# Kernel optimization log

Measured on AMD Instinct MI355X. Metric: run time of the kernel, lower is better.

Reference implementation:

```python
import jax, jax.numpy as jnp
import numpy as np


def _one_sided_chamfer(a, b):
    # a: [B, N, 3], b: [B, M, 3]
    # squared pairwise distances via ||a||^2 + ||b||^2 - 2 a.b
    a2 = jnp.sum(a * a, axis=-1)              # [B, N]
    b2 = jnp.sum(b * b, axis=-1)              # [B, M]
    ab = jnp.einsum('bnd,bmd->bnm', a, b)     # [B, N, M]
    d2 = a2[:, :, None] + b2[:, None, :] - 2.0 * ab
    d2 = jnp.maximum(d2, 0.0)                 # numerical floor
    # nearest neighbor in b for each point of a, averaged
    return jnp.mean(jnp.min(d2, axis=2))


def setup_inputs() -> dict:
    key = jax.random.key(0)
    k1, k2 = jax.random.split(key)
    B, N, D = 8, 8192, 3
    predict_pc = jax.random.normal(k1, (B, N, D), dtype=jnp.float32)
    gt_pc = jax.random.normal(k2, (B, N, D), dtype=jnp.float32)
    return {"predict_pc": predict_pc, "gt_pc": gt_pc}


def reference(predict_pc, gt_pc):
    dist1 = _one_sided_chamfer(predict_pc, gt_pc)
    dist2 = _one_sided_chamfer(gt_pc, predict_pc)
    return (dist1 + dist2) / 2.0
```

## Files before the change

### kernel.cpp

```cpp
#include <hip/hip_runtime.h>


#define BATCH   8
#define NPTS    8192
#define BLK     256
#define TOTAL_A (2 * BATCH * NPTS)
#define CHUNK   512
#define NCHUNK  (NPTS / CHUNK)
#define TPC     (CHUNK / 32)
#define ABLKS   (NPTS / 256)
#define P1_BLOCKS (2 * BATCH * ABLKS)
#define SC      16.0f

typedef _Float16 f16x8  __attribute__((ext_vector_type(8)));
typedef float    f32x16 __attribute__((ext_vector_type(16)));
typedef __attribute__((address_space(1))) const void gptr_t;
typedef __attribute__((address_space(3))) void lptr_t;

static __device__ __forceinline__ unsigned int pk2(float a, float b) {
  unsigned short ua = __builtin_bit_cast(unsigned short, (_Float16)a);
  unsigned short ub = __builtin_bit_cast(unsigned short, (_Float16)b);
  return (unsigned int)ua | ((unsigned int)ub << 16);
}

static __device__ __forceinline__ float fold16(float mq, f32x16 d) {
  float t0 = fmaxf(fmaxf(d[0],  d[1]),  d[2]);
  float t1 = fmaxf(fmaxf(d[3],  d[4]),  d[5]);
  float t2 = fmaxf(fmaxf(d[6],  d[7]),  d[8]);
  float t3 = fmaxf(fmaxf(d[9],  d[10]), d[11]);
  float t4 = fmaxf(fmaxf(d[12], d[13]), d[14]);
  float t5 = fmaxf(fmaxf(t0, t1), t2);
  float t6 = fmaxf(fmaxf(t3, t4), d[15]);
  return fmaxf(fmaxf(mq, t5), t6);
}

static __device__ __forceinline__ void fmt_point(float X, float Y, float Z,
                                                 uint4* lo, uint4* hi) {
  float x = X * SC, y = Y * SC, z = Z * SC;
  float fx = (float)(_Float16)x, fy = (float)(_Float16)y, fz = (float)(_Float16)z;
  float lx = x - fx, ly = y - fy, lz = z - fz;
  float b2 = fmaf(x, x, fmaf(y, y, z * z));
  float c  = -0.5f * b2;
  float fc = (float)(_Float16)c;
  float lc = c - fc;
  *lo = make_uint4(pk2(x, y), pk2(z, lx), pk2(ly, lz), pk2(x, y));
  *hi = make_uint4(pk2(z, c), pk2(lc, 1.0f), 0x00003C00u, 0u);
}

static __device__ __forceinline__ f16x8 make_afrag(float X, float Y, float Z,
                                                   int hi) {
  float x = X * SC, y = Y * SC, z = Z * SC;
  float fx = (float)(_Float16)x, fy = (float)(_Float16)y, fz = (float)(_Float16)z;
  float lx = x - fx, ly = y - fy, lz = z - fz;
  float a2 = fmaf(x, x, fmaf(y, y, z * z));
  float dd = -0.5f * a2;
  float fd = (float)(_Float16)dd;
  float ld = dd - fd;
  uint4 u;
  if (!hi) {
    u = make_uint4(pk2(x, y), pk2(z, x), pk2(y, z), pk2(lx, ly));
  } else {
    u = make_uint4(pk2(lz, 1.0f), pk2(1.0f, dd), pk2(ld, 0.0f), 0u);
  }
  return __builtin_bit_cast(f16x8, u);
}

__global__ __launch_bounds__(BLK) void chamfer_fmt(
    const float* __restrict__ pred, const float* __restrict__ gt,
    uint4* __restrict__ fmt, unsigned int* __restrict__ counter) {
  const int gid = blockIdx.x * BLK + threadIdx.x;
  if (gid == 0) *counter = 0u;
  const int arr = gid >> 16;
  const int idx = gid & 65535;
  const float* src = arr ? gt : pred;
  float X = src[(size_t)idx * 3 + 0];
  float Y = src[(size_t)idx * 3 + 1];
  float Z = src[(size_t)idx * 3 + 2];
  uint4 lo, hi;
  fmt_point(X, Y, Z, &lo, &hi);
  const int region = gid >> 13;
  const int p      = gid & 8191;
  size_t base = (size_t)region * 16384 + (size_t)(p >> 5) * 64 + (p & 31);
  fmt[base]      = lo;
  fmt[base + 32] = hi;
}

static __device__ __forceinline__ void stage_chunk(const uint4* src,
                                                   uint4* dst,
                                                   int wave, int lane) {
#pragma unroll
  for (int k = 0; k < 4; ++k) {
    const uint4* g = src + wave * 256 + k * 64 + lane;
    uint4*       l = dst + wave * 256 + k * 64;
    __builtin_amdgcn_global_load_lds((gptr_t*)g, (lptr_t*)l, 16, 0, 0);
  }
}

__global__ __launch_bounds__(BLK, 4) void chamfer_mfma_pass1(
    const float* __restrict__ pred, const float* __restrict__ gt,
    const uint4* __restrict__ fmt, float* __restrict__ blockSums,
    unsigned int* __restrict__ counter, float* __restrict__ out) {
  __shared__ uint4 lds4[2 * 1024];
  __shared__ float wsum[4];
  __shared__ int amLast;

  const int swz   = ((blockIdx.x & 7) << 6) | (blockIdx.x >> 3);
  const int ablk  = swz & (ABLKS - 1);
  const int bd    = swz >> 5;
  const int batch = bd & 7;
  const int side  = bd >> 3;

  const float* A    = side ? gt : pred;
  const uint4* fmtB = fmt + (size_t)((1 - side) * 8 + batch) * 16384;

  const int t    = threadIdx.x;
  const int lane = t & 63;
  const int wave = t >> 6;
  const int col  = lane & 31;
  const int hi   = lane >> 5;

  const float* Ab = A + ((size_t)batch * NPTS + (size_t)ablk * 256 + (size_t)wave * 64) * 3;
  f16x8 af0 = make_afrag(Ab[col * 3 + 0], Ab[col * 3 + 1], Ab[col * 3 + 2], hi);
  f16x8 af1 = make_afrag(Ab[(32 + col) * 3 + 0], Ab[(32 + col) * 3 + 1],
                         Ab[(32 + col) * 3 + 2], hi);
  float mq0 = -3.0e38f, mq1 = -3.0e38f;
  const f32x16 zero = {};

  stage_chunk(fmtB, lds4, wave, lane);
  __syncthreads();

  for (int c = 0; c < NCHUNK; ++c) {
    const uint4* rbuf = lds4 + (c & 1) * 1024;
    if (c + 1 < NCHUNK)
      stage_chunk(fmtB + (size_t)(c + 1) * 1024, lds4 + ((c + 1) & 1) * 1024,
                  wave, lane);

#pragma unroll
    for (int tt = 0; tt < TPC; ++tt) {
      f16x8 bf = *(const f16x8*)(rbuf + tt * 64 + lane);
      f32x16 d0 = __builtin_amdgcn_mfma_f32_32x32x16_f16(bf, af0, zero, 0, 0, 0);
      f32x16 d1 = __builtin_amdgcn_mfma_f32_32x32x16_f16(bf, af1, zero, 0, 0, 0);
      mq0 = fold16(mq0, d0);
      mq1 = fold16(mq1, d1);
    }
    __syncthreads();
  }

  mq0 = fmaxf(mq0, __shfl_xor(mq0, 32));
  mq1 = fmaxf(mq1, __shfl_xor(mq1, 32));

  float v = 0.0f;
  if (lane < 32) {
    float d20 = fmaxf(mq0 * (-1.0f / 128.0f), 0.0f);
    float d21 = fmaxf(mq1 * (-1.0f / 128.0f), 0.0f);
    v = d20 + d21;
  }
  for (int off = 32; off > 0; off >>= 1) v += __shfl_down(v, off);
  if (lane == 0) wsum[wave] = v;
  __syncthreads();
  if (t == 0) {
    float s = (wsum[0] + wsum[1]) + (wsum[2] + wsum[3]);
    blockSums[swz] = s;
    __threadfence();
    unsigned int prev = atomicAdd(counter, 1u);
    amLast = (prev == P1_BLOCKS - 1);
  }
  __syncthreads();

  if (amLast) {
    __threadfence();
    const volatile float* vbs = blockSums;
    float v2 = vbs[t] + vbs[t + 256];
    for (int off = 32; off > 0; off >>= 1) v2 += __shfl_down(v2, off);
    if (lane == 0) wsum[wave] = v2;
    __syncthreads();
    if (t == 0) {
      float s = ((wsum[0] + wsum[1]) + wsum[2]) + wsum[3];
      out[0] = s * (1.0f / (float)TOTAL_A);
    }
  }
}

extern "C" void kernel_launch(void* const* d_in, const int* in_sizes, int n_in,
                              void* d_out, int out_size, void* d_ws, size_t ws_size,
                              hipStream_t stream) {
  const float* pred = (const float*)d_in[0];
  const float* gt   = (const float*)d_in[1];
  float* out = (float*)d_out;

  uint4*        fmtb      = (uint4*)d_ws;
  float*        blockSums = (float*)((char*)d_ws + (size_t)TOTAL_A * 32);
  unsigned int* counter   = (unsigned int*)(blockSums + P1_BLOCKS);

  chamfer_fmt<<<TOTAL_A / BLK, BLK, 0, stream>>>(pred, gt, fmtb, counter);
  chamfer_mfma_pass1<<<P1_BLOCKS, BLK, 0, stream>>>(pred, gt, fmtb, blockSums,
                                                    counter, out);
}
```

Measured before the change: 104.1 us.

## Split B-point range into four quarters across blocks with separate reduction kernel

Each block now scans only a quarter of the opposite point cloud, so the grid grows from 512 to 2048 blocks. Per-point partial maxima go to a workspace array, and a new third kernel takes the max over the four partials, converts to distance, and does the final sum with a last-block reduction. LDS per block is halved and launch bounds raised to allow more resident blocks, which should fill the 256 CUs better than 512 blocks did. The cost is one extra kernel launch plus extra global traffic for the partials.

```diff
diff --git a/kernel.cpp b/kernel.cpp
--- a/kernel.cpp
+++ b/kernel.cpp
@@ -5,11 +5,14 @@
 #define NPTS    8192
 #define BLK     256
 #define TOTAL_A (2 * BATCH * NPTS)
-#define CHUNK   512
-#define NCHUNK  (NPTS / CHUNK)
+#define NCH4    4
+#define BQUART  (NPTS / NCH4)
+#define CHUNK   256
+#define NCHUNK  (BQUART / CHUNK)
 #define TPC     (CHUNK / 32)
 #define ABLKS   (NPTS / 256)
-#define P1_BLOCKS (2 * BATCH * ABLKS)
+#define P1_BLOCKS (2 * BATCH * ABLKS * NCH4)
+#define P2_BLOCKS (TOTAL_A / BLK)
 #define SC      16.0f
 
 typedef _Float16 f16x8  __attribute__((ext_vector_type(8)));
@@ -89,29 +92,29 @@
                                                    uint4* dst,
                                                    int wave, int lane) {
 #pragma unroll
-  for (int k = 0; k < 4; ++k) {
-    const uint4* g = src + wave * 256 + k * 64 + lane;
-    uint4*       l = dst + wave * 256 + k * 64;
+  for (int k = 0; k < 2; ++k) {
+    const uint4* g = src + wave * 128 + k * 64 + lane;
+    uint4*       l = dst + wave * 128 + k * 64;
     __builtin_amdgcn_global_load_lds((gptr_t*)g, (lptr_t*)l, 16, 0, 0);
   }
 }
 
-__global__ __launch_bounds__(BLK, 4) void chamfer_mfma_pass1(
+__global__ __launch_bounds__(BLK, 8) void chamfer_mfma_pass1(
     const float* __restrict__ pred, const float* __restrict__ gt,
-    const uint4* __restrict__ fmt, float* __restrict__ blockSums,
-    unsigned int* __restrict__ counter, float* __restrict__ out) {
-  __shared__ uint4 lds4[2 * 1024];
-  __shared__ float wsum[4];
-  __shared__ int amLast;
-
-  const int swz   = ((blockIdx.x & 7) << 6) | (blockIdx.x >> 3);
-  const int ablk  = swz & (ABLKS - 1);
-  const int bd    = swz >> 5;
+    const uint4* __restrict__ fmt, float* __restrict__ partial) {
+  __shared__ uint4 lds4[2 * 512];
+
+  const int swz   = ((blockIdx.x & 7) << 8) | (blockIdx.x >> 3);
+  const int qc    = swz & 3;
+  const int r     = swz >> 2;
+  const int ablk  = r & (ABLKS - 1);
+  const int bd    = r >> 5;
   const int batch = bd & 7;
   const int side  = bd >> 3;
 
   const float* A    = side ? gt : pred;
-  const uint4* fmtB = fmt + (size_t)((1 - side) * 8 + batch) * 16384;
+  const uint4* fmtB = fmt + (size_t)((1 - side) * 8 + batch) * 16384
+                          + (size_t)qc * 4096;
 
   const int t    = threadIdx.x;
   const int lane = t & 63;
@@ -130,9 +133,9 @@
   __syncthreads();
 
   for (int c = 0; c < NCHUNK; ++c) {
-    const uint4* rbuf = lds4 + (c & 1) * 1024;
+    const uint4* rbuf = lds4 + (c & 1) * 512;
     if (c + 1 < NCHUNK)
-      stage_chunk(fmtB + (size_t)(c + 1) * 1024, lds4 + ((c + 1) & 1) * 1024,
+      stage_chunk(fmtB + (size_t)(c + 1) * 512, lds4 + ((c + 1) & 1) * 512,
                   wave, lane);
 
 #pragma unroll
@@ -149,32 +152,46 @@
   mq0 = fmaxf(mq0, __shfl_xor(mq0, 32));
   mq1 = fmaxf(mq1, __shfl_xor(mq1, 32));
 
-  float v = 0.0f;
   if (lane < 32) {
-    float d20 = fmaxf(mq0 * (-1.0f / 128.0f), 0.0f);
-    float d21 = fmaxf(mq1 * (-1.0f / 128.0f), 0.0f);
-    v = d20 + d21;
-  }
+    size_t a0 = (size_t)bd * NPTS + (size_t)ablk * 256 + (size_t)wave * 64 + col;
+    partial[a0 * NCH4 + qc]        = mq0;
+    partial[(a0 + 32) * NCH4 + qc] = mq1;
+  }
+}
+
+__global__ __launch_bounds__(BLK) void chamfer_pass2fin(
+    const float4* __restrict__ partial, float* __restrict__ blockSums,
+    unsigned int* __restrict__ counter, float* __restrict__ out) {
+  __shared__ float wsum[BLK / 64];
+  __shared__ int amLast;
+
+  const int gid = blockIdx.x * BLK + threadIdx.x;
+  float4 p = partial[gid];
+  float m  = fmaxf(fmaxf(p.x, p.y), fmaxf(p.z, p.w));
+  float d2 = fmaxf(m * (-1.0f / 128.0f), 0.0f);
+
+  const int lane = threadIdx.x & 63, wave = threadIdx.x >> 6;
+  float v = d2;
   for (int off = 32; off > 0; off >>= 1) v += __shfl_down(v, off);
   if (lane == 0) wsum[wave] = v;
   __syncthreads();
-  if (t == 0) {
+  if (threadIdx.x == 0) {
     float s = (wsum[0] + wsum[1]) + (wsum[2] + wsum[3]);
-    blockSums[swz] = s;
+    blockSums[blockIdx.x] = s;
     __threadfence();
     unsigned int prev = atomicAdd(counter, 1u);
-    amLast = (prev == P1_BLOCKS - 1);
+    amLast = (prev == P2_BLOCKS - 1);
   }
   __syncthreads();
 
   if (amLast) {
     __threadfence();
     const volatile float* vbs = blockSums;
-    float v2 = vbs[t] + vbs[t + 256];
+    float v2 = vbs[threadIdx.x] + vbs[threadIdx.x + 256];
     for (int off = 32; off > 0; off >>= 1) v2 += __shfl_down(v2, off);
     if (lane == 0) wsum[wave] = v2;
     __syncthreads();
-    if (t == 0) {
+    if (threadIdx.x == 0) {
       float s = ((wsum[0] + wsum[1]) + wsum[2]) + wsum[3];
       out[0] = s * (1.0f / (float)TOTAL_A);
     }
@@ -189,10 +206,12 @@
   float* out = (float*)d_out;
 
   uint4*        fmtb      = (uint4*)d_ws;
-  float*        blockSums = (float*)((char*)d_ws + (size_t)TOTAL_A * 32);
-  unsigned int* counter   = (unsigned int*)(blockSums + P1_BLOCKS);
+  float*        partial   = (float*)((char*)d_ws + (size_t)TOTAL_A * 32);
+  float*        blockSums = partial + (size_t)TOTAL_A * NCH4;
+  unsigned int* counter   = (unsigned int*)(blockSums + P2_BLOCKS);
 
   chamfer_fmt<<<TOTAL_A / BLK, BLK, 0, stream>>>(pred, gt, fmtb, counter);
-  chamfer_mfma_pass1<<<P1_BLOCKS, BLK, 0, stream>>>(pred, gt, fmtb, blockSums,
-                                                    counter, out);
-}
+  chamfer_mfma_pass1<<<P1_BLOCKS, BLK, 0, stream>>>(pred, gt, fmtb, partial);
+  chamfer_pass2fin<<<P2_BLOCKS, BLK, 0, stream>>>((const float4*)partial,
+                                                  blockSums, counter, out);
+}
```

New measurement: 102.1 us. Within noise of the previous version (-1.9%).
